# Performance work log

Measured on AMD Instinct MI355X. Metric: run time of the kernel, lower is better.

The kernel has to match this reference:

```python
import jax, jax.numpy as jnp
import numpy as np

D_MODEL = 1024
NUM_HEADS = 16
SEG = 512            # segment_size
DIL = 4              # dilation_rate
HEAD_DIM = D_MODEL // NUM_HEADS


def setup_inputs() -> dict:
    key = jax.random.key(0)
    ks = jax.random.split(key, 5)
    B, S = 4, 4096
    sc = D_MODEL ** -0.5  # keep projected activations O(1) so softmax is not saturated
    def w(k):
        return jax.random.normal(k, (D_MODEL, D_MODEL), jnp.float32) * sc
    z = jnp.zeros((D_MODEL,), jnp.float32)
    return {
        "x": jax.random.normal(ks[0], (B, S, D_MODEL), jnp.float32),
        "Wq": w(ks[1]), "bq": z,
        "Wk": w(ks[2]), "bk": z,
        "Wv": w(ks[3]), "bv": z,
        "Wo": w(ks[4]), "bo": z,
    }


def reference(x, Wq, bq, Wk, bk, Wv, bv, Wo, bo):
    B, S, D = x.shape
    H, hd, seg, r = NUM_HEADS, HEAD_DIM, SEG, DIL
    scaling = hd ** -0.5

    Q = x @ Wq + bq
    K = x @ Wk + bk
    V = x @ Wv + bv

    pad = (-S) % seg
    if pad:
        Q = jnp.pad(Q, ((0, 0), (0, pad), (0, 0)))
        K = jnp.pad(K, ((0, 0), (0, pad), (0, 0)))
        V = jnp.pad(V, ((0, 0), (0, pad), (0, 0)))
    n = (S + pad) // seg          # num_segments
    sd = seg // r                 # dilated positions per segment per head

    # [B, n, sd, r, H, hd]: position within segment = t*r + offset
    def split(t):
        return t.reshape(B, n, sd, r, H, hd)

    offs = jnp.arange(H) % r      # per-head dilation offset sj = j % r
    hidx = jnp.arange(H)
    # vectorized per-head dilated gather -> [B, n, sd, H, hd]
    Qs = split(Q)[:, :, :, offs, hidx, :]
    Ks = split(K)[:, :, :, offs, hidx, :]
    Vs = split(V)[:, :, :, offs, hidx, :]

    # diagonal q.k score per dilated position, softmax over the segment's dilated positions
    scores = jnp.einsum('bnshd,bnshd->bnsh', Qs, Ks) * scaling
    probs = jax.nn.softmax(scores, axis=2)
    attn = probs[..., None] * Vs  # [B, n, sd, H, hd]

    # scatter back to each head's dilated positions; other positions stay zero
    out = jnp.zeros((B, n, sd, r, H, hd), x.dtype)
    out = out.at[:, :, :, offs, hidx, :].set(attn)
    out = out.reshape(B, n * seg, D)[:, :S]
    return out @ Wo + bo
```

## Files before the change

kernel.cpp:

```cpp
#include <hip/hip_runtime.h>
#include <hip/hip_bf16.h>

typedef unsigned short u16;
typedef unsigned int u32;
typedef __attribute__((ext_vector_type(8))) __bf16 bf16x8;
typedef __attribute__((ext_vector_type(4))) float f32x4;

#define NB 4
#define SQ 4096
#define DM 1024
#define RPC 4096
#define S4 (4 * DM)

#define VMCNT(n) asm volatile("s_waitcnt vmcnt(" #n ")" ::: "memory")
#define LGKM0()  asm volatile("s_waitcnt lgkmcnt(0)" ::: "memory")
#define BARRIER() asm volatile("s_barrier" ::: "memory")

__device__ __forceinline__ u16 f2b(float f) {
  u32 u = __builtin_bit_cast(u32, f);
  u32 r = u + 0x7fffu + ((u >> 16) & 1u);
  return (u16)(r >> 16);
}
__device__ __forceinline__ u32 cvt2(float lo, float hi) {
  u16 a = __builtin_bit_cast(u16, __float2bfloat16(lo));
  u16 b = __builtin_bit_cast(u16, __float2bfloat16(hi));
  return (u32)a | ((u32)b << 16);
}
__device__ __forceinline__ float dot2(u32 q, u32 k) {
  float ql = __builtin_bit_cast(float, q << 16);
  float qh = __builtin_bit_cast(float, q & 0xffff0000u);
  float kl = __builtin_bit_cast(float, k << 16);
  float kh = __builtin_bit_cast(float, k & 0xffff0000u);
  return ql * kl + qh * kh;
}
__device__ __forceinline__ u32 mul2(u32 v, float p) {
  float lo = __builtin_bit_cast(float, v << 16) * p;
  float hi = __builtin_bit_cast(float, v & 0xffff0000u) * p;
  return (u32)f2b(lo) | ((u32)f2b(hi) << 16);
}
__device__ __forceinline__ void gll16(const void* g, void* l) {
  __builtin_amdgcn_global_load_lds(
      (const __attribute__((address_space(1))) void*)g,
      (__attribute__((address_space(3))) void*)l, 16, 0, 0);
}

__global__ __launch_bounds__(256) void prep(const float* __restrict__ x,
                                            const float* __restrict__ Wq,
                                            const float* __restrict__ Wk,
                                            const float* __restrict__ Wv,
                                            const float* __restrict__ Wo,
                                            const float* __restrict__ bq,
                                            const float* __restrict__ bk,
                                            const float* __restrict__ bv,
                                            u16* __restrict__ xbT,
                                            u16* __restrict__ WTp,
                                            u16* __restrict__ WoTp,
                                            float* __restrict__ biasp) {
  __shared__ float T[64][65];
  const int bid = blockIdx.x;
  const int tid = threadIdx.x;
  if (bid < 1024) {
    const int wv = tid >> 6, l = tid & 63;
    const int gr0 = bid * 16 + wv * 4;
#pragma unroll
    for (int it = 0; it < 4; ++it) {
      const int gr = gr0 + it;
      const int c = gr >> 12, pr = gr & 4095;
      const int b = pr >> 10;
      const int srow = ((pr & 1023) << 2) + c;
      const int m0 = pr >> 8, rloc = pr & 255;
      const float* src = x + ((size_t)(b * SQ) + srow) * DM;
      u16* dimg = xbT + (size_t)((c * 16 + m0) * 16) * 16384 + rloc * 64;
      const int swzbase = ((((l & 15) >> 1) ^ (rloc & 7)) << 3) + (l & 1) * 4;
#pragma unroll
      for (int i = 0; i < 4; ++i) {
        float4 v = *reinterpret_cast<const float4*>(src + i * 256 + l * 4);
        uint2 pk;
        pk.x = cvt2(v.x, v.y);
        pk.y = cvt2(v.z, v.w);
        const int k64 = i * 4 + (l >> 4);
        *reinterpret_cast<uint2*>(dimg + (size_t)k64 * 16384 + swzbase) = pk;
      }
    }
  } else if (bid < 1792) {
    const int q = bid - 1024;
    const int c = q / 192;
    const int rem = q - c * 192;
    const int j0 = (rem >> 4) * 64;
    const int k0 = (rem & 15) * 64;
    const int msel = j0 >> 8;
    const float* W = (msel == 0) ? Wq : ((msel == 1) ? Wk : Wv);
    const int slot = (j0 & 255) >> 6;
    const int colbase = (c + 4 * slot) * 64;
    const int rr = tid >> 6, cc = tid & 63;
#pragma unroll
    for (int it = 0; it < 16; ++it) {
      const int kk = rr + it * 4;
      T[kk][cc] = W[(size_t)(k0 + kk) * 1024 + colbase + cc];
    }
    __syncthreads();
    const int k64 = k0 >> 6;
    const int u = cc >> 3, e = cc & 7;
#pragma unroll
    for (int it = 0; it < 16; ++it) {
      const int jj = rr + it * 4;
      const int j = j0 + jj;
      const int n0 = j / 192, nrow = j - n0 * 192;
      WTp[((size_t)((c * 4 + n0) * 16 + k64)) * 12288 + nrow * 64 + (((u ^ (nrow & 7))) << 3) + e] =
          f2b(T[cc][jj]);
    }
  } else if (bid < 2048) {
    const int q = bid - 1792;
    const int c = q >> 6;
    const int rem = q & 63;
    const int e0 = (rem >> 2) * 64;
    const int j0 = (rem & 3) * 64;
    const int rowbase = c * 64 + (j0 >> 6) * 256;
    const int rr = tid >> 6, cc = tid & 63;
#pragma unroll
    for (int it = 0; it < 16; ++it) {
      const int jj = rr + it * 4;
      T[jj][cc] = Wo[(size_t)(rowbase + jj) * 1024 + e0 + cc];
    }
    __syncthreads();
    const int k64 = j0 >> 6;
    const int u = cc >> 3, e = cc & 7;
#pragma unroll
    for (int it = 0; it < 16; ++it) {
      const int ee = rr + it * 4;
      const int n = e0 + ee;
      const int n0 = n >> 7, nrow = n & 127;
      WoTp[((size_t)((c * 8 + n0) * 4 + k64)) * 8192 + nrow * 64 + (((u ^ (nrow & 7))) << 3) + e] =
          f2b(T[cc][ee]);
    }
  } else {
    const int idx = (bid - 2048) * 256 + tid;
    if (idx < 3072) {
      const int c = idx / 768, j = idx % 768;
      const int msel = j >> 8, jj = j & 255;
      const int col = (c + 4 * (jj >> 6)) * 64 + (jj & 63);
      const float* bb = (msel == 0) ? bq : ((msel == 1) ? bk : bv);
      biasp[idx] = bb[col];
    }
  }
}

__global__ __launch_bounds__(256, 2) void gemm_qkv(const u16* __restrict__ xbT,
                                                   const u16* __restrict__ WTp,
                                                   const float* __restrict__ biasp,
                                                   u16* __restrict__ QKV) {
  __shared__ __align__(16) u16 As2[2 * 8192];
  __shared__ __align__(16) u16 Bs2[2 * 12288];
  const int p = blockIdx.x;
  const int L = (p & 7) * 64 + (p >> 3);
  const int c = L >> 7, r = L & 127;
  const int m0 = r >> 2, n0 = r & 3;
  const int tid = threadIdx.x;
  const int lane = tid & 63, w = tid >> 6;
  const int wm = w >> 1, wn = w & 1;
  const int l15 = lane & 15, l16 = lane >> 4;

  const u16* Asrc = xbT + (size_t)((c * 16 + (m0 >> 1)) * 16) * 16384 + (m0 & 1) * 8192;
  const u16* Bsrc = WTp + (size_t)((c * 4 + n0) * 16) * 12288;

  f32x4 acc[4][6];
#pragma unroll
  for (int i = 0; i < 4; ++i)
#pragma unroll
    for (int j = 0; j < 6; ++j) acc[i][j] = (f32x4){0.f, 0.f, 0.f, 0.f};

  int abase[2], bbase[2];
#pragma unroll
  for (int kk = 0; kk < 2; ++kk) {
    const int unit = kk * 4 + l16;
    abase[kk] = (wm * 64 + l15) * 64 + ((unit ^ (l15 & 7)) << 3);
    bbase[kk] = (wn * 96 + l15) * 64 + ((unit ^ (l15 & 7)) << 3);
  }

#define ISSUE_A(kt, buf)                                                   \
  {                                                                        \
    _Pragma("unroll") for (int i = 0; i < 4; ++i)                          \
        gll16(Asrc + (size_t)(kt) * 16384 + i * 2048 + tid * 8,            \
              (char*)As2 + (buf) * 16384 + i * 4096 + tid * 16);           \
  }
#define ISSUE_B(kt, buf)                                                   \
  {                                                                        \
    _Pragma("unroll") for (int i = 0; i < 6; ++i)                          \
        gll16(Bsrc + (size_t)(kt) * 12288 + i * 2048 + tid * 8,            \
              (char*)Bs2 + (buf) * 24576 + i * 4096 + tid * 16);           \
  }

  ISSUE_A(0, 0);
  ISSUE_B(0, 0);
  ISSUE_A(1, 1);
  ISSUE_B(1, 1);
  VMCNT(10);
  BARRIER();

#pragma unroll 1
  for (int t = 0; t < 16; ++t) {
    const u16* Ab = As2 + (t & 1) * 8192;
    const u16* Bb = Bs2 + (t & 1) * 12288;
#pragma unroll
    for (int kk = 0; kk < 2; ++kk) {
      bf16x8 af[4], bv[6];
#pragma unroll
      for (int mf = 0; mf < 4; ++mf)
        af[mf] = *reinterpret_cast<const bf16x8*>(Ab + abase[kk] + mf * 1024);
#pragma unroll
      for (int nf = 0; nf < 6; ++nf)
        bv[nf] = *reinterpret_cast<const bf16x8*>(Bb + bbase[kk] + nf * 1024);
      __builtin_amdgcn_s_setprio(1);
#pragma unroll
      for (int mf = 0; mf < 4; ++mf)
#pragma unroll
        for (int nf = 0; nf < 6; ++nf)
          acc[mf][nf] = __builtin_amdgcn_mfma_f32_16x16x32_bf16(af[mf], bv[nf], acc[mf][nf], 0, 0, 0);
      __builtin_amdgcn_s_setprio(0);
    }
    if (t == 15) break;
    BARRIER();
    if (t <= 13) {
      ISSUE_A(t + 2, t & 1);
      ISSUE_B(t + 2, t & 1);
      VMCNT(10);
    } else {
      VMCNT(0);
    }
    BARRIER();
  }
#undef ISSUE_A
#undef ISSUE_B

  const int rbase = m0 * 128;
  u16* outc = QKV + (size_t)c * RPC * 768;
#pragma unroll
  for (int mf = 0; mf < 4; ++mf) {
#pragma unroll
    for (int nf = 0; nf < 6; ++nf) {
      const int gcol = n0 * 192 + wn * 96 + nf * 16 + l15;
      const float bias = biasp[c * 768 + gcol];
#pragma unroll
      for (int jj = 0; jj < 4; ++jj) {
        const int rowt = wm * 64 + mf * 16 + l16 * 4 + jj;
        outc[(size_t)(rbase + rowt) * 768 + gcol] = f2b(acc[mf][nf][jj] + bias);
      }
    }
  }
}

__global__ __launch_bounds__(256, 2) void attn_out(const u16* __restrict__ QKV,
                                                   const u16* __restrict__ WoTp,
                                                   const float* __restrict__ bo,
                                                   float* __restrict__ out) {
  __shared__ __align__(16) u16 As2[2 * 8192];
  __shared__ __align__(16) u16 Bs2[2 * 8192];
  __shared__ float pL[512];
  const int p = blockIdx.x;
  const int xcd = p & 7, idx = p >> 3;
  const int cm = xcd * 16 + (idx >> 3);
  const int n0 = idx & 7;
  const int c = cm >> 5, m0 = cm & 31;
  const int tid = threadIdx.x;
  const int lane = tid & 63, w = tid >> 6;
  const int wm = w >> 1, wn = w & 1;
  const int l15 = lane & 15, l16 = lane >> 4;

  const u16* qkv = QKV + ((size_t)c * RPC + m0 * 128) * 768;
  const u16* Bsrc = WoTp + (size_t)((c * 8 + n0) * 4) * 8192;

#pragma unroll
  for (int it = 0; it < 2; ++it) {
    const int sidx = tid + it * 256;
    const int row = sidx & 127, slot = sidx >> 7;
    const u16* qp = qkv + (size_t)row * 768 + slot * 64;
    float s = 0.f;
#pragma unroll
    for (int dd = 0; dd < 8; ++dd) {
      uint4 qa = *reinterpret_cast<const uint4*>(qp + dd * 8);
      uint4 ka = *reinterpret_cast<const uint4*>(qp + 256 + dd * 8);
      s += dot2(qa.x, ka.x) + dot2(qa.y, ka.y) + dot2(qa.z, ka.z) + dot2(qa.w, ka.w);
    }
    pL[slot * 128 + row] = s * 0.125f;
  }
  __syncthreads();

  const int vrow = tid >> 1;
  const int vq = (tid & 1) * 32;
  const u16* vsrc = qkv + (size_t)vrow * 768 + 512 + vq;
  uint4 vv0, vv1, vv2, vv3;
#define LOADV(kt)                                                          \
  {                                                                        \
    vv0 = *reinterpret_cast<const uint4*>(vsrc + (kt) * 64);               \
    vv1 = *reinterpret_cast<const uint4*>(vsrc + (kt) * 64 + 8);           \
    vv2 = *reinterpret_cast<const uint4*>(vsrc + (kt) * 64 + 16);          \
    vv3 = *reinterpret_cast<const uint4*>(vsrc + (kt) * 64 + 24);          \
  }
#define ISSUE_BO(kt, buf)                                                  \
  {                                                                        \
    _Pragma("unroll") for (int i = 0; i < 4; ++i)                          \
        gll16(Bsrc + (size_t)(kt) * 8192 + i * 2048 + tid * 8,             \
              (char*)Bs2 + (buf) * 16384 + i * 4096 + tid * 16);           \
  }
  const int aw0 = vrow * 64 + ((((tid & 1) * 4) ^ (vrow & 7)) << 3);
  const int aw1 = vrow * 64 + (((((tid & 1) * 4) + 1) ^ (vrow & 7)) << 3);
  const int aw2 = vrow * 64 + (((((tid & 1) * 4) + 2) ^ (vrow & 7)) << 3);
  const int aw3 = vrow * 64 + (((((tid & 1) * 4) + 3) ^ (vrow & 7)) << 3);
#define WRITEA(kt, buf)                                                    \
  {                                                                        \
    const float pr = pL[(kt) * 128 + vrow];                                \
    u16* ab = As2 + (buf) * 8192;                                          \
    uint4 r0, r1, r2, r3;                                                  \
    r0.x = mul2(vv0.x, pr); r0.y = mul2(vv0.y, pr);                        \
    r0.z = mul2(vv0.z, pr); r0.w = mul2(vv0.w, pr);                        \
    r1.x = mul2(vv1.x, pr); r1.y = mul2(vv1.y, pr);                        \
    r1.z = mul2(vv1.z, pr); r1.w = mul2(vv1.w, pr);                        \
    r2.x = mul2(vv2.x, pr); r2.y = mul2(vv2.y, pr);                        \
    r2.z = mul2(vv2.z, pr); r2.w = mul2(vv2.w, pr);                        \
    r3.x = mul2(vv3.x, pr); r3.y = mul2(vv3.y, pr);                        \
    r3.z = mul2(vv3.z, pr); r3.w = mul2(vv3.w, pr);                        \
    *reinterpret_cast<uint4*>(ab + aw0) = r0;                              \
    *reinterpret_cast<uint4*>(ab + aw1) = r1;                              \
    *reinterpret_cast<uint4*>(ab + aw2) = r2;                              \
    *reinterpret_cast<uint4*>(ab + aw3) = r3;                              \
  }

  LOADV(0);
  ISSUE_BO(0, 0);
  ISSUE_BO(1, 1);

  {
    float* sv = &pL[w * 128];
    const float v0 = sv[lane], v1 = sv[lane + 64];
    float m = fmaxf(v0, v1);
#pragma unroll
    for (int off = 32; off; off >>= 1) m = fmaxf(m, __shfl_xor(m, off));
    const float e0 = __expf(v0 - m), e1 = __expf(v1 - m);
    float ssum = e0 + e1;
#pragma unroll
    for (int off = 32; off; off >>= 1) ssum += __shfl_xor(ssum, off);
    const float inv = 1.f / ssum;
    sv[lane] = e0 * inv;
    sv[lane + 64] = e1 * inv;
  }
  __syncthreads();

  f32x4 acc[4][4];
#pragma unroll
  for (int i = 0; i < 4; ++i)
#pragma unroll
    for (int j = 0; j < 4; ++j) acc[i][j] = (f32x4){0.f, 0.f, 0.f, 0.f};

  int aoff[2][4], boff[2][4];
#pragma unroll
  for (int kk = 0; kk < 2; ++kk) {
    const int unit = kk * 4 + l16;
#pragma unroll
    for (int f = 0; f < 4; ++f) {
      const int ra = wm * 64 + f * 16 + l15;
      aoff[kk][f] = ra * 64 + ((unit ^ (ra & 7)) << 3);
      const int rb = wn * 64 + f * 16 + l15;
      boff[kk][f] = rb * 64 + ((unit ^ (rb & 7)) << 3);
    }
  }

  VMCNT(8);
  WRITEA(0, 0);
  LOADV(1);
  VMCNT(8);
  LGKM0();
  BARRIER();

#pragma unroll 1
  for (int t = 0; t < 4; ++t) {
    const u16* Ab = As2 + (t & 1) * 8192;
    const u16* Bb = Bs2 + (t & 1) * 8192;
#pragma unroll
    for (int kk = 0; kk < 2; ++kk) {
      bf16x8 af[4], bvv[4];
#pragma unroll
      for (int f = 0; f < 4; ++f) {
        af[f] = *reinterpret_cast<const bf16x8*>(Ab + aoff[kk][f]);
        bvv[f] = *reinterpret_cast<const bf16x8*>(Bb + boff[kk][f]);
      }
      __builtin_amdgcn_s_setprio(1);
#pragma unroll
      for (int mf = 0; mf < 4; ++mf)
#pragma unroll
        for (int nf = 0; nf < 4; ++nf)
          acc[mf][nf] = __builtin_amdgcn_mfma_f32_16x16x32_bf16(af[mf], bvv[nf], acc[mf][nf], 0, 0, 0);
      __builtin_amdgcn_s_setprio(0);
    }
    if (t == 3) break;
    BARRIER();
    if (t <= 1) {
      ISSUE_BO(t + 2, t & 1);
      VMCNT(4);
    } else {
      VMCNT(0);
    }
    WRITEA(t + 1, (t + 1) & 1);
    if (t <= 1) LOADV(t + 2);
    LGKM0();
    BARRIER();
  }
#undef LOADV
#undef ISSUE_BO
#undef WRITEA

  const int rbase = m0 * 128;
  const int b = rbase >> 10;
  const int sbase = ((rbase & 1023) << 2) + c;
  float* outp = out + (size_t)(b * SQ + sbase) * DM;
#pragma unroll
  for (int mf = 0; mf < 4; ++mf) {
#pragma unroll
    for (int nf = 0; nf < 4; ++nf) {
      const int gcol = n0 * 128 + wn * 64 + nf * 16 + l15;
      const float bias = bo[gcol];
#pragma unroll
      for (int jj = 0; jj < 4; ++jj) {
        const int rowt = wm * 64 + mf * 16 + l16 * 4 + jj;
        outp[(size_t)rowt * S4 + gcol] = acc[mf][nf][jj] + bias;
      }
    }
  }
}

extern "C" void kernel_launch(void* const* d_in, const int* in_sizes, int n_in,
                              void* d_out, int out_size, void* d_ws, size_t ws_size,
                              hipStream_t stream) {
  const float* x  = (const float*)d_in[0];
  const float* Wq = (const float*)d_in[1];
  const float* bq = (const float*)d_in[2];
  const float* Wk = (const float*)d_in[3];
  const float* bk = (const float*)d_in[4];
  const float* Wv = (const float*)d_in[5];
  const float* bv = (const float*)d_in[6];
  const float* Wo = (const float*)d_in[7];
  const float* bo = (const float*)d_in[8];
  float* out = (float*)d_out;

  char* ws = (char*)d_ws;
  u16* xbT  = (u16*)(ws);
  u16* WoTp = (u16*)(ws + 33554432);
  u16* QKV  = (u16*)(ws + 35651584);

  char* ob = (char*)d_out;
  u16*   WTp   = (u16*)(ob + 33554432);
  float* biasp = (float*)(ob + 39845888);

  prep<<<2060, 256, 0, stream>>>(x, Wq, Wk, Wv, Wo, bq, bk, bv, xbT, WTp, WoTp, biasp);
  gemm_qkv<<<512, 256, 0, stream>>>(xbT, WTp, biasp, QKV);
  attn_out<<<1024, 256, 0, stream>>>(QKV, WoTp, bo, out);
}
```

Baseline: 92.65 us.

## Stage attn_out epilogue through LDS for coalesced float4 stores; lane-parallel score dots

```diff
diff --git a/kernel.cpp b/kernel.cpp
--- a/kernel.cpp
+++ b/kernel.cpp
@@ -253,9 +253,12 @@
                                                    const u16* __restrict__ WoTp,
                                                    const float* __restrict__ bo,
                                                    float* __restrict__ out) {
-  __shared__ __align__(16) u16 As2[2 * 8192];
-  __shared__ __align__(16) u16 Bs2[2 * 8192];
-  __shared__ float pL[512];
+  __shared__ __align__(16) char SMEM[67584];
+  u16* As2 = (u16*)SMEM;
+  u16* Bs2 = (u16*)(SMEM + 32768);
+  float* pL = (float*)(SMEM + 65536);
+  float* EP = (float*)SMEM;
+
   const int p = blockIdx.x;
   const int xcd = p & 7, idx = p >> 3;
   const int cm = xcd * 16 + (idx >> 3);
@@ -269,19 +272,21 @@
   const u16* qkv = QKV + ((size_t)c * RPC + m0 * 128) * 768;
   const u16* Bsrc = WoTp + (size_t)((c * 8 + n0) * 4) * 8192;
 
-#pragma unroll
-  for (int it = 0; it < 2; ++it) {
-    const int sidx = tid + it * 256;
-    const int row = sidx & 127, slot = sidx >> 7;
-    const u16* qp = qkv + (size_t)row * 768 + slot * 64;
-    float s = 0.f;
-#pragma unroll
-    for (int dd = 0; dd < 8; ++dd) {
-      uint4 qa = *reinterpret_cast<const uint4*>(qp + dd * 8);
-      uint4 ka = *reinterpret_cast<const uint4*>(qp + 256 + dd * 8);
-      s += dot2(qa.x, ka.x) + dot2(qa.y, ka.y) + dot2(qa.z, ka.z) + dot2(qa.w, ka.w);
-    }
-    pL[slot * 128 + row] = s * 0.125f;
+  {
+    const int g = lane >> 3, dd = lane & 7;
+#pragma unroll 4
+    for (int it = 0; it < 16; ++it) {
+      const int P = it * 32 + w * 8 + g;
+      const int row = P >> 2, slot = P & 3;
+      const u16* qp = qkv + (size_t)row * 768 + slot * 64 + dd * 8;
+      uint4 qa = *reinterpret_cast<const uint4*>(qp);
+      uint4 ka = *reinterpret_cast<const uint4*>(qp + 256);
+      float s = dot2(qa.x, ka.x) + dot2(qa.y, ka.y) + dot2(qa.z, ka.z) + dot2(qa.w, ka.w);
+      s += __shfl_xor(s, 1);
+      s += __shfl_xor(s, 2);
+      s += __shfl_xor(s, 4);
+      if (dd == 0) pL[slot * 128 + row] = s * 0.125f;
+    }
   }
   __syncthreads();
 
@@ -408,21 +413,36 @@
 #undef ISSUE_BO
 #undef WRITEA
 
-  const int rbase = m0 * 128;
-  const int b = rbase >> 10;
-  const int sbase = ((rbase & 1023) << 2) + c;
-  float* outp = out + (size_t)(b * SQ + sbase) * DM;
+  LGKM0();
+  BARRIER();
 #pragma unroll
   for (int mf = 0; mf < 4; ++mf) {
 #pragma unroll
     for (int nf = 0; nf < 4; ++nf) {
-      const int gcol = n0 * 128 + wn * 64 + nf * 16 + l15;
-      const float bias = bo[gcol];
+      const int col = wn * 64 + nf * 16 + l15;
 #pragma unroll
       for (int jj = 0; jj < 4; ++jj) {
         const int rowt = wm * 64 + mf * 16 + l16 * 4 + jj;
-        outp[(size_t)rowt * S4 + gcol] = acc[mf][nf][jj] + bias;
+        EP[rowt * 130 + col] = acc[mf][nf][jj];
       }
+    }
+  }
+  LGKM0();
+  BARRIER();
+  {
+    const int col4 = lane & 31;
+    const int rsub = lane >> 5;
+    const float4 bo4 = *reinterpret_cast<const float4*>(bo + n0 * 128 + col4 * 4);
+    const int rbase = m0 * 128;
+    const int b = rbase >> 10;
+    const int sbase = ((rbase & 1023) << 2) + c;
+    float* outp = out + (size_t)(b * SQ + sbase) * DM + n0 * 128;
+#pragma unroll
+    for (int i = 0; i < 16; ++i) {
+      const int row = w * 2 + rsub + i * 8;
+      float4 v = *reinterpret_cast<const float4*>(&EP[row * 130 + col4 * 4]);
+      v.x += bo4.x; v.y += bo4.y; v.z += bo4.z; v.w += bo4.w;
+      *reinterpret_cast<float4*>(outp + (size_t)row * S4 + col4 * 4) = v;
     }
   }
 }
```

New measurement: 96.11 us. +3.7%, slower.
